# Performance work log

Hardware: AMD Instinct MI355X
Metric: run time of the kernel (lower is better)

The kernel has to match this reference:

```python
import jax, jax.numpy as jnp
from jax import lax
import numpy as np
import math

NUM_CLASSES = 1
IOU_THR = 0.5
SCORE_THR = 0.05
MAX_DET = 300
IMG_H = IMG_W = 640


def _base_anchors(base_size, ratios, scales):
    n = len(ratios) * len(scales)
    a = np.zeros((n, 4))
    a[:, 2:] = base_size * np.tile(scales, (2, len(ratios))).T
    areas = a[:, 2] * a[:, 3]
    a[:, 2] = np.sqrt(areas / np.repeat(ratios, len(scales)))
    a[:, 3] = a[:, 2] * np.repeat(ratios, len(scales))
    a[:, 0::2] -= np.tile(a[:, 2] * 0.5, (2, 1)).T
    a[:, 1::2] -= np.tile(a[:, 3] * 0.5, (2, 1)).T
    return a


def build_anchors(H, W):
    # standard RetinaNet anchors: levels 3..7, 3 ratios x 3 scales
    ratios = np.array([0.5, 1.0, 2.0])
    scales = np.array([2.0 ** 0, 2.0 ** (1.0 / 3.0), 2.0 ** (2.0 / 3.0)])
    out = []
    for l in (3, 4, 5, 6, 7):
        stride, base = 2 ** l, 2 ** (l + 2)
        ba = _base_anchors(base, ratios, scales)  # (9,4)
        fh, fw = (H + stride - 1) // stride, (W + stride - 1) // stride
        sx = (np.arange(fw) + 0.5) * stride
        sy = (np.arange(fh) + 0.5) * stride
        xx, yy = np.meshgrid(sx, sy)  # (fh, fw) row-major over (y, x) -> matches head NHWC flatten
        shifts = np.stack([xx.ravel(), yy.ravel(), xx.ravel(), yy.ravel()], 1)
        out.append((shifts[:, None, :] + ba[None, :, :]).reshape(-1, 4))
    return jnp.asarray(np.concatenate(out, 0), jnp.float32)


def conv3x3(x, w, b):
    y = lax.conv_general_dilated(x, w, (1, 1), 'SAME', dimension_numbers=('NCHW', 'OIHW', 'NCHW'))
    return y + b[None, :, None, None]


def run_head(feat, ws, bs, ow, ob):
    h = feat
    for k in range(ws.shape[0]):  # 4 shared conv+relu layers
        h = jax.nn.relu(conv3x3(h, ws[k], bs[k]))
    return conv3x3(h, ow, ob)


def decode_boxes(anchors, reg):
    w = anchors[:, 2] - anchors[:, 0]
    h = anchors[:, 3] - anchors[:, 1]
    cx = anchors[:, 0] + 0.5 * w
    cy = anchors[:, 1] + 0.5 * h
    pcx = cx + reg[:, 0] * 0.1 * w
    pcy = cy + reg[:, 1] * 0.1 * h
    pw = jnp.exp(reg[:, 2] * 0.2) * w
    ph = jnp.exp(reg[:, 3] * 0.2) * h
    return jnp.stack([pcx - 0.5 * pw, pcy - 0.5 * ph, pcx + 0.5 * pw, pcy + 0.5 * ph], 1)


def greedy_nms(boxes, scores):
    # fixed-size greedy NMS (jit-safe stand-in for torchvision.ops.nms), capped at MAX_DET
    s0 = jnp.where(scores > SCORE_THR, scores, -jnp.inf)
    areas = (boxes[:, 2] - boxes[:, 0]) * (boxes[:, 3] - boxes[:, 1])

    def body(i, carry):
        s, out_s, out_b = carry
        j = jnp.argmax(s)
        sj = s[j]
        keep = sj > -jnp.inf
        bj = boxes[j]
        xx1 = jnp.maximum(bj[0], boxes[:, 0])
        yy1 = jnp.maximum(bj[1], boxes[:, 1])
        xx2 = jnp.minimum(bj[2], boxes[:, 2])
        yy2 = jnp.minimum(bj[3], boxes[:, 3])
        inter = jnp.maximum(xx2 - xx1, 0.0) * jnp.maximum(yy2 - yy1, 0.0)
        iou = inter / (areas + areas[j] - inter + 1e-8)
        s = jnp.where(iou > IOU_THR, -jnp.inf, s)  # self-IoU == 1 also removes j
        out_s = out_s.at[i].set(jnp.where(keep, sj, 0.0))
        out_b = out_b.at[i].set(jnp.where(keep, bj, jnp.zeros((4,), boxes.dtype)))
        return s, out_s, out_b

    init = (s0, jnp.zeros((MAX_DET,), boxes.dtype), jnp.zeros((MAX_DET, 4), boxes.dtype))
    _, out_s, out_b = lax.fori_loop(0, MAX_DET, body, init)
    return out_s, out_b


def forward(img, feats, cls_w, cls_b, cls_ow, cls_ob, reg_w, reg_b, reg_ow, reg_ob):
    B = feats[0].shape[0]
    cls_list, reg_list = [], []
    for f in feats:
        c = run_head(f, cls_w, cls_b, cls_ow, cls_ob)  # [B, 9*C, h, w]
        cls_list.append(jnp.transpose(c, (0, 2, 3, 1)).reshape(B, -1, NUM_CLASSES))
        r = run_head(f, reg_w, reg_b, reg_ow, reg_ob)  # [B, 36, h, w]
        reg_list.append(jnp.transpose(r, (0, 2, 3, 1)).reshape(B, -1, 4))
    classification = jax.nn.sigmoid(jnp.concatenate(cls_list, 1))  # [B, N, C]
    regression = jnp.concatenate(reg_list, 1)                      # [B, N, 4]
    H, W = img.shape[2], img.shape[3]
    anchors = build_anchors(H, W)
    boxes = decode_boxes(anchors, regression[0])
    boxes = jnp.clip(boxes, jnp.zeros((4,), boxes.dtype), jnp.asarray([W, H, W, H], boxes.dtype))
    all_s, all_l, all_b = [], [], []
    for i in range(NUM_CLASSES):  # static per-class loop, mirrors eager loop
        s, b = greedy_nms(boxes, classification[0, :, i])
        all_s.append(s)
        all_b.append(b)
        all_l.append(jnp.where(s > 0.0, i, -1))
    return jnp.concatenate(all_s), jnp.concatenate(all_l), jnp.concatenate(all_b, 0)


def setup_inputs():
    key = jax.random.key(0)
    ks = jax.random.split(key, 16)
    C = 256
    scale = 0.03  # ~He std for 3x3x256 fan-in; keeps head activations O(1)
    sizes = [(80, 80), (40, 40), (20, 20), (10, 10), (5, 5)]
    inp = {'img': jnp.zeros((1, 3, IMG_H, IMG_W), jnp.float32)}
    for i, (name, (h, w)) in enumerate(zip(['p3', 'p4', 'p5', 'p6', 'p7'], sizes)):
        inp[name] = jax.random.normal(ks[i], (1, C, h, w), jnp.float32)
    na = 9
    bias_init = -math.log((1.0 - 0.01) / 0.01)  # prior_probability = 0.01
    inp['cls_w'] = jax.random.normal(ks[5], (4, C, C, 3, 3), jnp.float32) * scale
    inp['cls_b'] = jnp.zeros((4, C), jnp.float32)
    inp['cls_ow'] = jax.random.normal(ks[6], (na * NUM_CLASSES, C, 3, 3), jnp.float32) * scale
    inp['cls_ob'] = jnp.full((na * NUM_CLASSES,), bias_init, jnp.float32)
    inp['reg_w'] = jax.random.normal(ks[7], (4, C, C, 3, 3), jnp.float32) * scale
    inp['reg_b'] = jnp.zeros((4, C), jnp.float32)
    inp['reg_ow'] = jax.random.normal(ks[8], (na * 4, C, 3, 3), jnp.float32) * scale
    inp['reg_ob'] = jnp.zeros((na * 4,), jnp.float32)
    return inp


def reference(img, p3, p4, p5, p6, p7, cls_w, cls_b, cls_ow, cls_ob, reg_w, reg_b, reg_ow, reg_ob):
    return forward(img, (p3, p4, p5, p6, p7), cls_w, cls_b, cls_ow, cls_ob, reg_w, reg_b, reg_ow, reg_ob)
```

## Files before the change

kernel.cpp:

```cpp
#include <hip/hip_runtime.h>
#include <math.h>

#define N_ANCH 76725
#define SORT_N 4096
#define NBKT 1024
#define BBASE 0x3D40u

typedef _Float16 f16;
typedef _Float16 f16x8 __attribute__((ext_vector_type(8)));
typedef float f32x4 __attribute__((ext_vector_type(4)));

__device__ __forceinline__ int pick5(int l, int a, int b, int c, int d, int e) {
  int r = a;
  if (l == 1) r = b;
  if (l == 2) r = c;
  if (l == 3) r = d;
  if (l == 4) r = e;
  return r;
}

__device__ __forceinline__ void tile_to_level(int tile, int& lvl, int& t) {
  int l = 0;
  if (tile >= 100) l = 1;
  if (tile >= 125) l = 2;
  if (tile >= 134) l = 3;
  if (tile >= 138) l = 4;
  lvl = l;
  t = tile - pick5(l, 0, 100, 125, 134, 138);
}

__device__ __forceinline__ int tile64_lvl(int bx, int& t) {
  int l = 0;
  if (bx >= 100) l = 1;
  if (bx >= 125) l = 2;
  if (bx >= 132) l = 3;
  if (bx >= 134) l = 4;
  t = bx - pick5(l, 0, 100, 125, 132, 134);
  return l;
}

__device__ __forceinline__ void split16(float v, f16& h, f16& l) {
  f16 hh = (f16)v;
  if (fabsf(v) < 6.103515625e-5f) hh = (f16)0.f;
  h = hh;
  l = (f16)((v - (float)hh) * 4096.f);
}

__device__ __forceinline__ void glds16h(const void* g, void* l) {
  __builtin_amdgcn_global_load_lds(
      (const __attribute__((address_space(1))) unsigned int*)g,
      (__attribute__((address_space(3))) unsigned int*)l, 16, 0, 0);
}

__device__ __forceinline__ void glds16(const float* g, float* l) {
  __builtin_amdgcn_global_load_lds(
      (const __attribute__((address_space(1))) unsigned int*)g,
      (__attribute__((address_space(3))) unsigned int*)l, 16, 0, 0);
}

struct FcvArgs {
  const float* f[5];
  f16* hi;
  f16* lo;
  unsigned short* zbuf;
};

__global__ __launch_bounds__(256) void featcvt_k(FcvArgs a) {
  __shared__ float tile[32][65];
  int t;
  const int l = tile64_lvl(blockIdx.x, t);
  const int W = 80 >> l, HW = W * W;
  const int p0 = t * 64;
  const int apos = pick5(l, 0, 6400, 8000, 8400, 8500);
  const int ci0 = blockIdx.y * 32;
  const int tid = threadIdx.x;
  if (blockIdx.x == 0 && blockIdx.y == 0 && tid < 32) a.zbuf[tid] = 0;
  const float* __restrict__ src = a.f[l];
  #pragma unroll
  for (int i = 0; i < 8; i++) {
    const int j = tid + 256 * i;
    const int ci = j >> 6, p = j & 63;
    float v = 0.f;
    if (p0 + p < HW) v = src[(ci0 + ci) * HW + p0 + p];
    tile[ci][p] = v;
  }
  __syncthreads();
  const int p_l = tid >> 2, cq = tid & 3;
  if (p0 + p_l < HW) {
    union { f16 h[8]; uint4 v; } uh, ul;
    #pragma unroll
    for (int u = 0; u < 8; u++) split16(tile[cq * 8 + u][p_l], uh.h[u], ul.h[u]);
    const size_t base = (size_t)(apos + p0 + p_l) * 256 + ci0 + cq * 8;
    *(uint4*)(a.hi + base) = uh.v;
    *(uint4*)(a.lo + base) = ul.v;
  }
}

__global__ __launch_bounds__(256) void wsplit_k(const float* __restrict__ src,
                                                f16* __restrict__ whi,
                                                f16* __restrict__ wlo) {
  const int e = blockIdx.x * 256 + threadIdx.x;
  const int k = e & 31, co = (e >> 5) & 255, c = e >> 13;
  const int tap = c >> 3, ciq = c & 7;
  const int ci = ciq * 32 + k;
  const float v = src[((size_t)co * 256 + ci) * 9 + tap];
  f16 h, lo;
  split16(v, h, lo);
  whi[e] = h;
  wlo[e] = lo;
}

struct WtrArgs {
  const float* src[2];
  float* dst;
};

__global__ __launch_bounds__(256) void wtr_k(WtrArgs a) {
  __shared__ float tile[72][65];
  const int r0 = blockIdx.x * 72;
  const int cog = blockIdx.y;
  const int co0 = cog * 64;
  const int head = blockIdx.z;
  const float* __restrict__ src = a.src[head];
  float* __restrict__ dst = a.dst + ((size_t)(head * 4 + cog) * 2304 + r0) * 64;
  const int tid = threadIdx.x;
  #pragma unroll
  for (int i = 0; i < 18; i++) {
    int e = tid + 256 * i;
    int co = e / 72;
    int r = e - co * 72;
    tile[r][co] = src[(size_t)(co0 + co) * 2304 + r0 + r];
  }
  __syncthreads();
  #pragma unroll
  for (int i = 0; i < 18; i++) {
    int e = tid + 256 * i;
    int r = e >> 6;
    int co = e & 63;
    dst[(size_t)r * 64 + co] = tile[r][co];
  }
}

__device__ __forceinline__ void a_load(const float* __restrict__ in, int ci0,
                                       int ty0, int tx0, int W, int HW, int tid,
                                       float a_reg[6]) {
  const float* inc = in + ci0 * HW;
  #pragma unroll
  for (int i = 0; i < 6; i++) {
    int e = tid + 256 * i;
    float v = 0.f;
    if (e < 1440) {
      int ci = e / 180;
      int rem = e - ci * 180;
      int yy = rem / 10;
      int xx = rem - yy * 10;
      int gy = ty0 + yy - 1, gx = tx0 + xx - 1;
      if ((unsigned)gy < (unsigned)W && (unsigned)gx < (unsigned)W)
        v = inc[ci * HW + gy * W + gx];
    }
    a_reg[i] = v;
  }
}

__device__ __forceinline__ void a_store(int tid, const float a_reg[6],
                                        float As[8][18][12]) {
  #pragma unroll
  for (int i = 0; i < 6; i++) {
    int e = tid + 256 * i;
    if (e < 1440) {
      int ci = e / 180;
      int rem = e - ci * 180;
      int yy = rem / 10;
      int xx = rem - yy * 10;
      As[ci][yy][xx] = a_reg[i];
    }
  }
}

__device__ __forceinline__ void stage_w(const float* __restrict__ wchunk,
                                        float* wbuf, int wv, int lane) {
  #pragma unroll
  for (int i = 0; i < 5; i++) {
    int j = wv + 4 * i;
    if (j < 18) glds16(wchunk + j * 256 + lane * 4, wbuf + j * 256);
  }
}

struct FusedArgs {
  const f16* in_hi;
  const f16* in_lo;
  const f16* w_hi;
  const f16* w_lo;
  float* acc0;
  float* acc1;
  const f16* zbuf;
  const float* cin[5];
  float* cout[5];
  const float* cw;
  const float* cb;
};

__global__ __launch_bounds__(256, 2) void fused_trunk(FusedArgs a) {
  __shared__ __align__(16) char smem[65536];
  const int bx = blockIdx.x;
  const int tid = threadIdx.x;
  if (bx < 296) {
    f16 (*Xh)[4096] = (f16 (*)[4096])(smem);
    f16 (*Xl)[4096] = (f16 (*)[4096])(smem + 16384);
    f16 (*Wh)[4096] = (f16 (*)[4096])(smem + 32768);
    f16 (*Wl)[4096] = (f16 (*)[4096])(smem + 49152);
    const int combo = bx & 3, tl = bx >> 2;
    const int cog = combo >> 1, kh = combo & 1;
    int l = 0;
    if (tl >= 50) l = 1;
    if (tl >= 65) l = 2;
    if (tl >= 71) l = 3;
    if (tl >= 73) l = 4;
    const int t = tl - pick5(l, 0, 50, 65, 71, 73);
    const int W = 80 >> l, HW = W * W, tX = (W + 7) >> 3;
    const int ty0 = (t / tX) * 16, tx0 = (t % tX) * 8;
    const int apos = pick5(l, 0, 6400, 8000, 8400, 8500);
    const int co0 = cog * 128;
    const int lane = tid & 63, wv = tid >> 6;
    const int ln15 = lane & 15, lh = lane >> 4;
    const int wco = wv & 1, wpos = wv >> 1;
    const f16* __restrict__ ihi = a.in_hi;
    const f16* __restrict__ ilo = a.in_lo;
    const f16* __restrict__ whi = a.w_hi;
    const f16* __restrict__ wlo = a.w_lo;

    f32x4 accA[4][4] = {};
    f32x4 accB[4][4] = {};

    auto stage = [&](int c, int buf) {
      const int tap = c >> 3, ciq = c & 7;
      const int dy = tap / 3 - 1, dx = tap - (tap / 3) * 3 - 1;
      #pragma unroll
      for (int i = 0; i < 2; i++) {
        const int s = (wv * 2 + i) * 64 + lane;
        const int pos = s >> 2, kq = s & 3;
        const int kqd = kq ^ (pos & 3);
        const int gy = ty0 + (pos >> 3) + dy, gx = tx0 + (pos & 7) + dx;
        const bool v = (unsigned)gy < (unsigned)W && (unsigned)gx < (unsigned)W;
        const int off = (apos + gy * W + gx) * 256 + ciq * 32 + kqd * 8;
        glds16h(v ? (const void*)(ihi + off) : (const void*)a.zbuf, &Xh[buf][(wv * 2 + i) * 512]);
        glds16h(v ? (const void*)(ilo + off) : (const void*)a.zbuf, &Xl[buf][(wv * 2 + i) * 512]);
      }
      const f16* wh = whi + (size_t)c * 8192;
      const f16* wl = wlo + (size_t)c * 8192;
      #pragma unroll
      for (int i = 0; i < 2; i++) {
        const int s = (wv * 2 + i) * 64 + lane;
        const int col = s >> 2, kq = s & 3;
        const int kqd = kq ^ (col & 3);
        const int off = (co0 + col) * 32 + kqd * 8;
        glds16h(wh + off, &Wh[buf][(wv * 2 + i) * 512]);
        glds16h(wl + off, &Wl[buf][(wv * 2 + i) * 512]);
      }
    };

    const int c0 = kh * 36;
    stage(c0, 0);
    __syncthreads();
    for (int j = 0; j < 36; j++) {
      const int b = j & 1;
      if (j < 35) stage(c0 + j + 1, b ^ 1);
      const int slot = (lh ^ (ln15 & 3)) * 8;
      const int aro = (wco * 64 + ln15) * 32 + slot;
      const int bro = (wpos * 64 + ln15) * 32 + slot;
      f16x8 ah[4], al[4];
      #pragma unroll
      for (int mi = 0; mi < 4; mi++) {
        ah[mi] = *(const f16x8*)&Wh[b][aro + mi * 512];
        al[mi] = *(const f16x8*)&Wl[b][aro + mi * 512];
      }
      #pragma unroll
      for (int ni = 0; ni < 4; ni++) {
        const f16x8 bhv = *(const f16x8*)&Xh[b][bro + ni * 512];
        const f16x8 blv = *(const f16x8*)&Xl[b][bro + ni * 512];
        #pragma unroll
        for (int mi = 0; mi < 4; mi++) {
          accA[mi][ni] = __builtin_amdgcn_mfma_f32_16x16x32_f16(ah[mi], bhv, accA[mi][ni], 0, 0, 0);
          accB[mi][ni] = __builtin_amdgcn_mfma_f32_16x16x32_f16(ah[mi], blv, accB[mi][ni], 0, 0, 0);
          accB[mi][ni] = __builtin_amdgcn_mfma_f32_16x16x32_f16(al[mi], bhv, accB[mi][ni], 0, 0, 0);
        }
      }
      __syncthreads();
    }

    const int aoffF = pick5(l, 0, 1638400, 2048000, 2150400, 2176000);
    float* __restrict__ dst = (kh == 0 ? a.acc0 : a.acc1) + aoffF;
    #pragma unroll
    for (int ni = 0; ni < 4; ni++) {
      const int pos = wpos * 64 + ni * 16 + ln15;
      const int gy = ty0 + (pos >> 3), gx = tx0 + (pos & 7);
      if (gy < W && gx < W) {
        #pragma unroll
        for (int mi = 0; mi < 4; mi++) {
          const int co = co0 + wco * 64 + mi * 16 + lh * 4;
          float* d = dst + (size_t)co * HW + gy * W + gx;
          #pragma unroll
          for (int r = 0; r < 4; r++)
            d[(size_t)r * HW] = accA[mi][ni][r] + accB[mi][ni][r] * 2.44140625e-4f;
        }
      }
    }
  } else {
    float (*As)[8][18][12] = (float (*)[8][18][12])(smem);
    float (*Ws)[72][64] = (float (*)[72][64])(smem + 13824);
    const int idx = bx - 296;
    const int cog = idx & 3;
    const int tl = idx >> 2;
    int l = 0;
    if (tl >= 50) l = 1;
    if (tl >= 65) l = 2;
    if (tl >= 71) l = 3;
    if (tl >= 73) l = 4;
    const int lvl = l;
    const int t = tl - pick5(l, 0, 50, 65, 71, 73);
    const int W = 80 >> lvl;
    const int HW = W * W;
    const int tX = (W + 7) >> 3;
    const int ty0 = (t / tX) * 16, tx0 = (t % tX) * 8;
    const int co0 = cog << 6;
    const float* __restrict__ in = a.cin[lvl];
    float* __restrict__ out = a.cout[lvl];
    const float* __restrict__ wsrc = a.cw + (size_t)cog * 2304 * 64;
    const int lane = tid & 63, wv = tid >> 6;
    const int cop = tid & 15;
    const int ry = tid >> 4;
    const int co_sub = cop << 2;
    float acc[8][4] = {};
    float a_reg[6];

    stage_w(wsrc, &Ws[0][0][0], wv, lane);
    a_load(in, 0, ty0, tx0, W, HW, tid, a_reg);
    a_store(tid, a_reg, As[0]);
    __syncthreads();

    for (int k = 0; k < 32; k++) {
      const int kb = k & 1;
      const bool more = k < 31;
      if (more) {
        stage_w(wsrc + (size_t)(k + 1) * 4608, &Ws[kb ^ 1][0][0], wv, lane);
        a_load(in, (k + 1) * 8, ty0, tx0, W, HW, tid, a_reg);
      }
      #pragma unroll 2
      for (int ci = 0; ci < 8; ci++) {
        #pragma unroll
        for (int ty = 0; ty < 3; ty++) {
          const float* ar = &As[kb][ci][ry + ty][0];
          float4 a0 = *(const float4*)ar;
          float4 a1 = *(const float4*)(ar + 4);
          float2 a2 = *(const float2*)(ar + 8);
          float av[10] = {a0.x, a0.y, a0.z, a0.w, a1.x, a1.y, a1.z, a1.w, a2.x, a2.y};
          #pragma unroll
          for (int tx = 0; tx < 3; tx++) {
            const float* wr = &Ws[kb][ci * 9 + ty * 3 + tx][co_sub];
            float4 wvv = *(const float4*)wr;
            #pragma unroll
            for (int p = 0; p < 8; p++) {
              acc[p][0] = fmaf(av[tx + p], wvv.x, acc[p][0]);
              acc[p][1] = fmaf(av[tx + p], wvv.y, acc[p][1]);
              acc[p][2] = fmaf(av[tx + p], wvv.z, acc[p][2]);
              acc[p][3] = fmaf(av[tx + p], wvv.w, acc[p][3]);
            }
          }
        }
      }
      if (more) {
        a_store(tid, a_reg, As[kb ^ 1]);
        __syncthreads();
      }
    }
    const float4 bias = *(const float4*)&a.cb[co0 + co_sub];
    const int oy = ty0 + ry;
    if (oy < W) {
      #pragma unroll
      for (int p = 0; p < 8; p++) {
        int ox = tx0 + p;
        if (ox < W) {
          int base = oy * W + ox;
          out[(co0 + co_sub + 0) * HW + base] = fmaxf(acc[p][0] + bias.x, 0.f);
          out[(co0 + co_sub + 1) * HW + base] = fmaxf(acc[p][1] + bias.y, 0.f);
          out[(co0 + co_sub + 2) * HW + base] = fmaxf(acc[p][2] + bias.z, 0.f);
          out[(co0 + co_sub + 3) * HW + base] = fmaxf(acc[p][3] + bias.w, 0.f);
        }
      }
    }
  }
}

struct EpiArgs {
  float* a0;
  const float* a1;
  const float* bias;
  f16* hi;
  f16* lo;
  int last;
};

__global__ __launch_bounds__(256) void epi_k(EpiArgs a) {
  __shared__ float tile[32][65];
  int t;
  const int l = tile64_lvl(blockIdx.x, t);
  const int W = 80 >> l, HW = W * W;
  const int p0 = t * 64;
  const int apos = pick5(l, 0, 6400, 8000, 8400, 8500);
  const int ci0 = blockIdx.y * 32;
  const int tid = threadIdx.x;
  float* __restrict__ s0 = a.a0 + (size_t)apos * 256;
  const float* __restrict__ s1 = a.a1 + (size_t)apos * 256;
  const float* __restrict__ bias = a.bias;
  #pragma unroll
  for (int i = 0; i < 8; i++) {
    const int j = tid + 256 * i;
    const int ci = j >> 6, p = j & 63;
    float v = 0.f;
    if (p0 + p < HW) {
      const size_t off = (size_t)(ci0 + ci) * HW + p0 + p;
      float x = s0[off];
      float y = s1[off];
      v = x + y;
    }
    tile[ci][p] = fmaxf(v + bias[ci0 + ci], 0.f);
  }
  __syncthreads();
  if (a.last) {
    #pragma unroll
    for (int i = 0; i < 8; i++) {
      const int j = tid + 256 * i;
      const int ci = j >> 6, p = j & 63;
      if (p0 + p < HW) s0[(size_t)(ci0 + ci) * HW + p0 + p] = tile[ci][p];
    }
  } else {
    const int p_l = tid >> 2, cq = tid & 3;
    if (p0 + p_l < HW) {
      union { f16 h[8]; uint4 v; } uh, ul;
      #pragma unroll
      for (int u = 0; u < 8; u++) split16(tile[cq * 8 + u][p_l], uh.h[u], ul.h[u]);
      const size_t base = (size_t)(apos + p0 + p_l) * 256 + ci0 + cq * 8;
      *(uint4*)(a.hi + base) = uh.v;
      *(uint4*)(a.lo + base) = ul.v;
    }
  }
}

struct Out2Args {
  const float* in[2][5];
  const float* w;
  const float* b[2];
  float* dst[2];
};

__global__ __launch_bounds__(256) void wtro_k(const float* __restrict__ cls_ow,
                                              const float* __restrict__ reg_ow,
                                              float* __restrict__ dst) {
  int r = blockIdx.x * 256 + threadIdx.x;
  if (r >= 2304) return;
  for (int g = 0; g < 5; g++) {
    #pragma unroll
    for (int s = 0; s < 16; s++) {
      int w = s >> 2, c = s & 3;
      float v = 0.f;
      if (w < 3 && c < 3) {
        int cl = 3 * w + c;
        v = (g == 0) ? cls_ow[(size_t)cl * 2304 + r]
                     : reg_ow[(size_t)((g - 1) * 9 + cl) * 2304 + r];
      }
      dst[((size_t)g * 2304 + r) * 16 + s] = v;
    }
  }
}

__device__ __forceinline__ void ao_load(const float* __restrict__ in, int ci0,
                                        int ty0, int tx0, int W, int HW, int tid,
                                        float a_reg[5]) {
  const float* inc = in + ci0 * HW;
  #pragma unroll
  for (int i = 0; i < 5; i++) {
    int e = tid + 192 * i;
    float v = 0.f;
    if (e < 800) {
      int ci = e / 100;
      int rem = e - ci * 100;
      int yy = rem / 10;
      int xx = rem - yy * 10;
      int gy = ty0 + yy - 1, gx = tx0 + xx - 1;
      if ((unsigned)gy < (unsigned)W && (unsigned)gx < (unsigned)W)
        v = inc[ci * HW + gy * W + gx];
    }
    a_reg[i] = v;
  }
}

__device__ __forceinline__ void ao_store(int tid, const float a_reg[5],
                                         float As[8][10][12]) {
  #pragma unroll
  for (int i = 0; i < 5; i++) {
    int e = tid + 192 * i;
    if (e < 800) {
      int ci = e / 100;
      int rem = e - ci * 100;
      int yy = rem / 10;
      int xx = rem - yy * 10;
      As[ci][yy][xx] = a_reg[i];
    }
  }
}

__global__ __launch_bounds__(192) void conv_out2(Out2Args args) {
  __shared__ float As[2][8][10][12];
  __shared__ __align__(16) float Wg[2][8][9][16];
  int lvl, t;
  tile_to_level(blockIdx.x, lvl, t);
  const int g = blockIdx.y;
  const int head = (g == 0) ? 0 : 1;
  const int co0 = (g == 0) ? 0 : (g - 1) * 9;
  const int W = 80 >> lvl;
  const int HW = W * W;
  const int tX = (W + 7) >> 3;
  const int ty0 = (t / tX) * 8, tx0 = (t % tX) * 8;
  const float* __restrict__ in = args.in[head][lvl];
  const float* __restrict__ wg = args.w + (size_t)g * 2304 * 16;
  const int tid = threadIdx.x;
  const int wv = tid >> 6;
  const int lane = tid & 63;
  const int y = lane >> 3, x = lane & 7;
  float acc0 = 0.f, acc1 = 0.f, acc2 = 0.f;
  float a_reg[5];
  float4 w_reg[2];

  ao_load(in, 0, ty0, tx0, W, HW, tid, a_reg);
  {
    const float4* wsrc4 = (const float4*)wg;
    #pragma unroll
    for (int i = 0; i < 2; i++) {
      int e = tid + 192 * i;
      if (e < 288) w_reg[i] = wsrc4[e];
    }
  }
  ao_store(tid, a_reg, As[0]);
  {
    float4* wdst4 = (float4*)&Wg[0][0][0][0];
    #pragma unroll
    for (int i = 0; i < 2; i++) {
      int e = tid + 192 * i;
      if (e < 288) wdst4[e] = w_reg[i];
    }
  }
  __syncthreads();

  for (int k = 0; k < 32; k++) {
    const int kb = k & 1;
    const bool more = k < 31;
    if (more) {
      ao_load(in, (k + 1) * 8, ty0, tx0, W, HW, tid, a_reg);
      const float4* wsrc4 = (const float4*)(wg + (size_t)(k + 1) * 1152);
      #pragma unroll
      for (int i = 0; i < 2; i++) {
        int e = tid + 192 * i;
        if (e < 288) w_reg[i] = wsrc4[e];
      }
    }
    #pragma unroll 2
    for (int ci = 0; ci < 8; ci++) {
      #pragma unroll
      for (int ty = 0; ty < 3; ty++) {
        float a0 = As[kb][ci][y + ty][x + 0];
        float a1 = As[kb][ci][y + ty][x + 1];
        float a2 = As[kb][ci][y + ty][x + 2];
        #pragma unroll
        for (int tx = 0; tx < 3; tx++) {
          float av = (tx == 0) ? a0 : (tx == 1) ? a1 : a2;
          float4 w4 = *(const float4*)&Wg[kb][ci][ty * 3 + tx][4 * wv];
          acc0 = fmaf(av, w4.x, acc0);
          acc1 = fmaf(av, w4.y, acc1);
          acc2 = fmaf(av, w4.z, acc2);
        }
      }
    }
    if (more) {
      ao_store(tid, a_reg, As[kb ^ 1]);
      float4* wdst4 = (float4*)&Wg[kb ^ 1][0][0][0];
      #pragma unroll
      for (int i = 0; i < 2; i++) {
        int e = tid + 192 * i;
        if (e < 288) wdst4[e] = w_reg[i];
      }
      __syncthreads();
    }
  }
  const int oy = ty0 + y, ox = tx0 + x;
  if (oy < W && ox < W) {
    const int cell = oy * W + ox;
    const int aoff = pick5(lvl, 0, 57600, 72000, 75600, 76500);
    float* dst = args.dst[head];
    const float* bias = args.b[head];
    #pragma unroll
    for (int c = 0; c < 3; c++) {
      int co = co0 + 3 * wv + c;
      float v = ((c == 0) ? acc0 : (c == 1) ? acc1 : acc2) + bias[co];
      if (head == 0) {
        v = 1.f / (1.f + expf(-v));
        dst[aoff + cell * 9 + co] = v;
      } else {
        dst[(size_t)aoff * 4 + cell * 36 + co] = v;
      }
    }
  }
}

__global__ void init_k(int* meta) {
  int i = blockIdx.x * 256 + threadIdx.x;
  if (i < 1 + NBKT) meta[i] = 0;
}

__global__ __launch_bounds__(256) void decode_k(const float* __restrict__ scores,
                                                const float* __restrict__ regs,
                                                float* cand_s, float4* cand_b,
                                                int* cand_n, int* meta) {
  int n = blockIdx.x * 256 + threadIdx.x;
  if (n >= N_ANCH) return;
  int lvl = 0;
  if (n >= 57600) lvl = 1;
  if (n >= 72000) lvl = 2;
  if (n >= 75600) lvl = 3;
  if (n >= 76500) lvl = 4;
  const int aoff = pick5(lvl, 0, 57600, 72000, 75600, 76500);
  const int W = 80 >> lvl;
  int r = n - aoff;
  int a = r % 9;
  int cell = r / 9;
  int x = cell % W, y = cell / W;
  double stride = (double)(8 << lvl);
  double base = (double)(32 << lvl);
  int si = a % 3, ri = a / 3;
  double s = (si == 0) ? 1.0 : (si == 1) ? 1.2599210498948731648 : 1.5874010519681994748;
  double ratio = (ri == 0) ? 0.5 : (ri == 1) ? 1.0 : 2.0;
  double ws0 = base * s;
  double area = ws0 * ws0;
  double w = sqrt(area / ratio);
  double h = w * ratio;
  double cx = ((double)x + 0.5) * stride;
  double cy = ((double)y + 0.5) * stride;
  float ax1 = (float)(cx - 0.5 * w);
  float ay1 = (float)(cy - 0.5 * h);
  float ax2 = (float)(cx + (w - 0.5 * w));
  float ay2 = (float)(cy + (h - 0.5 * h));
  float4 rg = ((const float4*)regs)[n];
  float aw = ax2 - ax1, ah = ay2 - ay1;
  float acx = ax1 + 0.5f * aw, acy = ay1 + 0.5f * ah;
  float pcx = acx + rg.x * 0.1f * aw;
  float pcy = acy + rg.y * 0.1f * ah;
  float pw = expf(rg.z * 0.2f) * aw;
  float ph = expf(rg.w * 0.2f) * ah;
  float x1 = pcx - 0.5f * pw, y1 = pcy - 0.5f * ph;
  float x2 = pcx + 0.5f * pw, y2 = pcy + 0.5f * ph;
  x1 = fminf(fmaxf(x1, 0.f), 640.f);
  y1 = fminf(fmaxf(y1, 0.f), 640.f);
  x2 = fminf(fmaxf(x2, 0.f), 640.f);
  y2 = fminf(fmaxf(y2, 0.f), 640.f);
  float sc = scores[n];
  if (sc > 0.05f) {
    int p = atomicAdd(&meta[0], 1);
    cand_s[p] = sc;
    cand_b[p] = make_float4(x1, y1, x2, y2);
    cand_n[p] = n;
    unsigned int sb = __float_as_uint(sc);
    int bk = (int)(sb >> 16) - (int)BBASE;
    bk = max(0, min(NBKT - 1, bk));
    atomicAdd(&meta[1 + bk], 1);
  }
}

__global__ __launch_bounds__(1024) void nms2_k(const float* __restrict__ cs,
                                               const float4* __restrict__ cb,
                                               const int* __restrict__ cn,
                                               const int* __restrict__ meta,
                                               float* __restrict__ out) {
  __shared__ unsigned long long skey[SORT_N];
  __shared__ int sidx[SORT_N];
  __shared__ int suf[NBKT];
  __shared__ float kx1[300], ky1[300], kx2[300], ky2[300], kar[300];
  __shared__ int sh_i[8];
  const int tid = threadIdx.x;
  const int m = min(meta[0], N_ANCH);

  for (int b = tid; b < NBKT; b += 1024) suf[b] = meta[1 + b];
  __syncthreads();
  for (int off = 1; off < NBKT; off <<= 1) {
    int v0 = suf[tid] + ((tid + off < NBKT) ? suf[tid + off] : 0);
    __syncthreads();
    suf[tid] = v0;
    __syncthreads();
  }

  int nk = 0;
  unsigned long long hi64 = ~0ULL;
  int processed = 0;

  while (nk < 300 && processed < m) {
    int base = 0;
    if (hi64 != ~0ULL) {
      if (tid == 0) sh_i[4] = 0;
      __syncthreads();
      int c = 0;
      for (int j = tid; j < m; j += 1024) {
        unsigned long long K = ((unsigned long long)__float_as_uint(cs[j]) << 32) |
                               (unsigned int)(~cn[j]);
        if (K >= hi64) c++;
      }
      atomicAdd(&sh_i[4], c);
      __syncthreads();
      base = sh_i[4];
      __syncthreads();
    }
    if (tid == 0) sh_i[3] = NBKT + 1;
    __syncthreads();
    {
      int T = tid;
      unsigned long long lo =
          (T == 0) ? 0ULL : ((unsigned long long)(((unsigned)T + BBASE) << 16) << 32);
      int c = suf[T] - base;
      if (lo < hi64 && c >= 1 && c <= SORT_N) atomicMin(&sh_i[3], T);
    }
    __syncthreads();
    int T = sh_i[3];
    __syncthreads();
    unsigned long long lo64;
    if (T <= NBKT) {
      lo64 = (T == 0) ? 0ULL : ((unsigned long long)(((unsigned)T + BBASE) << 16) << 32);
    } else {
      unsigned long long L = 0, H = hi64;
      while (H - L > 1) {
        unsigned long long mid = L + ((H - L) >> 1);
        if (tid == 0) sh_i[4] = 0;
        __syncthreads();
        int c = 0;
        for (int j = tid; j < m; j += 1024) {
          unsigned long long K = ((unsigned long long)__float_as_uint(cs[j]) << 32) |
                                 (unsigned int)(~cn[j]);
          if (K >= mid && K < hi64) c++;
        }
        atomicAdd(&sh_i[4], c);
        __syncthreads();
        int cc = sh_i[4];
        __syncthreads();
        if (cc > SORT_N) L = mid; else H = mid;
      }
      lo64 = H;
    }
    if (tid == 0) sh_i[0] = 0;
    __syncthreads();
    for (int j = tid; j < m; j += 1024) {
      unsigned long long K = ((unsigned long long)__float_as_uint(cs[j]) << 32) |
                             (unsigned int)(~cn[j]);
      if (K >= lo64 && K < hi64) {
        int p = atomicAdd(&sh_i[0], 1);
        if (p < SORT_N) { skey[p] = K; sidx[p] = j; }
      }
    }
    __syncthreads();
    int bn = min(sh_i[0], SORT_N);
    __syncthreads();
    for (int p = bn + tid; p < SORT_N; p += 1024) { skey[p] = 0; sidx[p] = 0; }
    __syncthreads();
    for (int k = 2; k <= SORT_N; k <<= 1) {
      for (int jj = k >> 1; jj > 0; jj >>= 1) {
        for (int i = tid; i < SORT_N; i += 1024) {
          int l2 = i ^ jj;
          if (l2 > i) {
            unsigned long long a = skey[i], b2 = skey[l2];
            bool desc = ((i & k) == 0);
            if ((a < b2) == desc) {
              skey[i] = b2; skey[l2] = a;
              int t2 = sidx[i]; sidx[i] = sidx[l2]; sidx[l2] = t2;
            }
          }
        }
        __syncthreads();
      }
    }
    {
      char* pool = (char*)skey;
      float* cx1 = (float*)pool;
      float* cy1 = cx1 + 256;
      float* cx2 = cy1 + 256;
      float* cy2 = cx2 + 256;
      float* car = cy2 + 256;
      int* sup = (int*)(car + 256);
      unsigned long long* msk = (unsigned long long*)(pool + 6144);
      int cpos = 0;
      while (cpos < bn && nk < 300) {
        const int cl = min(256, bn - cpos);
        if (tid < 256) sup[tid] = 0;
        if (tid < cl) {
          float4 b = cb[sidx[cpos + tid]];
          cx1[tid] = b.x; cy1[tid] = b.y; cx2[tid] = b.z; cy2[tid] = b.w;
          car[tid] = (b.z - b.x) * (b.w - b.y);
        }
        __syncthreads();
        {
          const int i = tid >> 2, q = tid & 3;
          if (i < cl) {
            const float bx1 = cx1[i], by1 = cy1[i], bx2 = cx2[i], by2 = cy2[i], ba = car[i];
            int flag = 0;
            for (int k2 = q; k2 < nk; k2 += 4) {
              float xx1 = fmaxf(kx1[k2], bx1), yy1 = fmaxf(ky1[k2], by1);
              float xx2 = fminf(kx2[k2], bx2), yy2 = fminf(ky2[k2], by2);
              float inter = fmaxf(xx2 - xx1, 0.f) * fmaxf(yy2 - yy1, 0.f);
              if (inter / (ba + kar[k2] - inter + 1e-8f) > 0.5f) { flag = 1; break; }
            }
            if (flag) atomicOr(&sup[i], 1);
          }
        }
        {
          const int i = tid >> 2, w = tid & 3;
          unsigned long long bits = 0ull;
          if (i < cl) {
            const float ax1 = cx1[i], ay1 = cy1[i], ax2 = cx2[i], ay2 = cy2[i], aa = car[i];
            const int j0 = w * 64;
            for (int jj = 0; jj < 64; jj++) {
              const int j2 = j0 + jj;
              if (j2 > i && j2 < cl) {
                float xx1 = fmaxf(ax1, cx1[j2]), yy1 = fmaxf(ay1, cy1[j2]);
                float xx2 = fminf(ax2, cx2[j2]), yy2 = fminf(ay2, cy2[j2]);
                float inter = fmaxf(xx2 - xx1, 0.f) * fmaxf(yy2 - yy1, 0.f);
                if (inter / (car[j2] + aa - inter + 1e-8f) > 0.5f) bits |= (1ull << jj);
              }
            }
          }
          msk[(tid >> 2) * 4 + (tid & 3)] = bits;
        }
        __syncthreads();
        if (tid == 0) {
          unsigned long long r0 = 0, r1 = 0, r2 = 0, r3 = 0;
          int lnk = nk;
          for (int i = 0; i < cl && lnk < 300; i++) {
            const unsigned long long rw = (i < 64) ? r0 : (i < 128) ? r1 : (i < 192) ? r2 : r3;
            if (sup[i] || ((rw >> (i & 63)) & 1ull)) continue;
            const float b1 = cx1[i], b2 = cy1[i], b3 = cx2[i], b4 = cy2[i];
            kx1[lnk] = b1; ky1[lnk] = b2; kx2[lnk] = b3; ky2[lnk] = b4; kar[lnk] = car[i];
            out[lnk] = cs[sidx[cpos + i]];
            out[300 + lnk] = 0.0f;
            out[600 + 4 * lnk + 0] = b1;
            out[600 + 4 * lnk + 1] = b2;
            out[600 + 4 * lnk + 2] = b3;
            out[600 + 4 * lnk + 3] = b4;
            lnk++;
            r0 |= msk[i * 4 + 0]; r1 |= msk[i * 4 + 1];
            r2 |= msk[i * 4 + 2]; r3 |= msk[i * 4 + 3];
          }
          sh_i[5] = lnk;
        }
        __syncthreads();
        nk = sh_i[5];
        cpos += cl;
        __syncthreads();
      }
    }
    processed = base + bn;
    hi64 = lo64;
  }
  __syncthreads();
  for (int r = nk + tid; r < 300; r += 1024) {
    out[r] = 0.f;
    out[300 + r] = -1.f;
    out[600 + 4 * r + 0] = 0.f;
    out[600 + 4 * r + 1] = 0.f;
    out[600 + 4 * r + 2] = 0.f;
    out[600 + 4 * r + 3] = 0.f;
  }
}

extern "C" void kernel_launch(void* const* d_in, const int* in_sizes, int n_in,
                              void* d_out, int out_size, void* d_ws, size_t ws_size,
                              hipStream_t stream) {
  (void)in_sizes; (void)n_in; (void)out_size; (void)ws_size;
  const float* feats[5];
  for (int ll = 0; ll < 5; ll++) feats[ll] = (const float*)d_in[1 + ll];
  const float* cls_w = (const float*)d_in[6];
  const float* cls_b = (const float*)d_in[7];
  const float* cls_ow = (const float*)d_in[8];
  const float* cls_ob = (const float*)d_in[9];
  const float* reg_w = (const float*)d_in[10];
  const float* reg_b = (const float*)d_in[11];
  const float* reg_ow = (const float*)d_in[12];
  const float* reg_ob = (const float*)d_in[13];

  static const int AOFF[5] = {0, 1638400, 2048000, 2150400, 2176000};
  const size_t ACT = 2182400;
  const size_t PLH = 2182400;

  float* wsf = (float*)d_ws;
  float* ACC0 = wsf;
  float* ACC1 = wsf + ACT;
  float* clsA = wsf + 2 * ACT;
  float* clsB = wsf + 3 * ACT;
  f16* slotA = (f16*)(wsf + 4 * ACT);
  f16* slotB = (f16*)(wsf + 5 * ACT);
  float* wt = wsf + 6 * ACT;
  f16* wpkh = (f16*)(wsf + 6 * ACT + 589824);
  f16* wpkl = (f16*)(wsf + 6 * ACT + 884736);
  unsigned short* zbuf = (unsigned short*)(wsf + 6 * ACT + 1179648);
  float* scores = wsf + 6 * ACT + 1179664;
  float* regs = scores + 76736;
  float* cand_s = regs + 306912;
  float* cand_b = cand_s + 76736;
  int* cand_n = (int*)(cand_b + 306944);
  int* meta = cand_n + 76736;
  float* wt2o = (float*)(meta + 1032);

  FcvArgs fa;
  for (int ll = 0; ll < 5; ll++) fa.f[ll] = feats[ll];
  fa.hi = slotB;
  fa.lo = slotB + PLH;
  fa.zbuf = zbuf;
  featcvt_k<<<dim3(135, 8), dim3(256), 0, stream>>>(fa);
  wtro_k<<<dim3(9), dim3(256), 0, stream>>>(cls_ow, reg_ow, wt2o);

  float* clsBufs[2] = {clsA, clsB};
  for (int layer = 0; layer < 4; layer++) {
    wsplit_k<<<dim3(2304), dim3(256), 0, stream>>>(reg_w + (size_t)layer * 589824, wpkh, wpkl);
    WtrArgs wa;
    wa.src[0] = cls_w + (size_t)layer * 589824;
    wa.src[1] = wa.src[0];
    wa.dst = wt;
    wtr_k<<<dim3(32, 4, 1), dim3(256), 0, stream>>>(wa);

    FusedArgs fu;
    if (layer == 0) {
      fu.in_hi = slotB;
      fu.in_lo = slotB + PLH;
    } else {
      f16* s = (layer & 1) ? slotA : slotB;
      fu.in_hi = s;
      fu.in_lo = s + PLH;
    }
    fu.w_hi = wpkh;
    fu.w_lo = wpkl;
    fu.acc0 = ACC0;
    fu.acc1 = ACC1;
    fu.zbuf = (const f16*)zbuf;
    fu.cw = wt;
    fu.cb = cls_b + layer * 256;
    for (int ll = 0; ll < 5; ll++) {
      fu.cout[ll] = clsBufs[layer & 1] + AOFF[ll];
      fu.cin[ll] = (layer == 0) ? feats[ll]
                                : (const float*)(clsBufs[(layer - 1) & 1] + AOFF[ll]);
    }
    fused_trunk<<<dim3(592), dim3(256), 0, stream>>>(fu);

    EpiArgs ea;
    f16* outS = (layer & 1) ? slotB : slotA;
    ea.a0 = ACC0;
    ea.a1 = ACC1;
    ea.bias = reg_b + layer * 256;
    ea.hi = outS;
    ea.lo = outS + PLH;
    ea.last = (layer == 3) ? 1 : 0;
    epi_k<<<dim3(135, 8), dim3(256), 0, stream>>>(ea);
  }

  Out2Args oa;
  for (int ll = 0; ll < 5; ll++) {
    oa.in[0][ll] = clsB + AOFF[ll];
    oa.in[1][ll] = ACC0 + AOFF[ll];
  }
  oa.w = wt2o;
  oa.b[0] = cls_ob;
  oa.b[1] = reg_ob;
  oa.dst[0] = scores;
  oa.dst[1] = regs;
  conv_out2<<<dim3(139, 5), dim3(192), 0, stream>>>(oa);

  init_k<<<dim3(5), dim3(256), 0, stream>>>(meta);
  decode_k<<<dim3((N_ANCH + 255) / 256), dim3(256), 0, stream>>>(scores, regs, cand_s,
                                                                 (float4*)cand_b, cand_n, meta);
  nms2_k<<<dim3(1), dim3(1024), 0, stream>>>(cand_s, (const float4*)cand_b, cand_n, meta,
                                             (float*)d_out);
}
```

Measured before the change: 1.422 ms.

## Hoist weight prep out of layer loop and split cls conv blocks finer

All four layers' weight split and transpose now run in one launch each before the layer loop, removing eight small launches from the loop. The fp32 cls-head conv blocks now cover 32 output channels and half-width columns instead of 64, and fused_trunk grows from 592 to 888 blocks. Cls and reg blocks are interleaved in a 1:2 ratio so the two kinds of work mix across CUs. Each cls block does less work with fewer accumulator registers, which adds parallelism but reloads activations twice as often and stores less reuse per block.

```diff
diff --git a/kernel.cpp b/kernel.cpp
--- a/kernel.cpp
+++ b/kernel.cpp
@@ -96,22 +96,24 @@
   }
 }
 
-__global__ __launch_bounds__(256) void wsplit_k(const float* __restrict__ src,
+__global__ __launch_bounds__(256) void wsplit_k(const float* __restrict__ reg_w,
                                                 f16* __restrict__ whi,
                                                 f16* __restrict__ wlo) {
   const int e = blockIdx.x * 256 + threadIdx.x;
+  const int layer = blockIdx.y;
+  const float* src = reg_w + (size_t)layer * 589824;
   const int k = e & 31, co = (e >> 5) & 255, c = e >> 13;
   const int tap = c >> 3, ciq = c & 7;
   const int ci = ciq * 32 + k;
   const float v = src[((size_t)co * 256 + ci) * 9 + tap];
   f16 h, lo;
   split16(v, h, lo);
-  whi[e] = h;
-  wlo[e] = lo;
+  whi[(size_t)layer * 589824 + e] = h;
+  wlo[(size_t)layer * 589824 + e] = lo;
 }
 
 struct WtrArgs {
-  const float* src[2];
+  const float* src;
   float* dst;
 };
 
@@ -120,9 +122,9 @@
   const int r0 = blockIdx.x * 72;
   const int cog = blockIdx.y;
   const int co0 = cog * 64;
-  const int head = blockIdx.z;
-  const float* __restrict__ src = a.src[head];
-  float* __restrict__ dst = a.dst + ((size_t)(head * 4 + cog) * 2304 + r0) * 64;
+  const int layer = blockIdx.z;
+  const float* __restrict__ src = a.src + (size_t)layer * 589824;
+  float* __restrict__ dst = a.dst + (size_t)layer * 589824 + ((size_t)cog * 2304 + r0) * 64;
   const int tid = threadIdx.x;
   #pragma unroll
   for (int i = 0; i < 18; i++) {
@@ -177,15 +179,6 @@
   }
 }
 
-__device__ __forceinline__ void stage_w(const float* __restrict__ wchunk,
-                                        float* wbuf, int wv, int lane) {
-  #pragma unroll
-  for (int i = 0; i < 5; i++) {
-    int j = wv + 4 * i;
-    if (j < 18) glds16(wchunk + j * 256 + lane * 4, wbuf + j * 256);
-  }
-}
-
 struct FusedArgs {
   const f16* in_hi;
   const f16* in_lo;
@@ -204,12 +197,14 @@
   __shared__ __align__(16) char smem[65536];
   const int bx = blockIdx.x;
   const int tid = threadIdx.x;
-  if (bx < 296) {
+  const int q3 = bx / 3, r3 = bx - q3 * 3;
+  if (r3 == 0) {
     f16 (*Xh)[4096] = (f16 (*)[4096])(smem);
     f16 (*Xl)[4096] = (f16 (*)[4096])(smem + 16384);
     f16 (*Wh)[4096] = (f16 (*)[4096])(smem + 32768);
     f16 (*Wl)[4096] = (f16 (*)[4096])(smem + 49152);
-    const int combo = bx & 3, tl = bx >> 2;
+    const int rb = q3;
+    const int combo = rb & 3, tl = rb >> 2;
     const int cog = combo >> 1, kh = combo & 1;
     int l = 0;
     if (tl >= 50) l = 1;
@@ -307,10 +302,10 @@
     }
   } else {
     float (*As)[8][18][12] = (float (*)[8][18][12])(smem);
-    float (*Ws)[72][64] = (float (*)[72][64])(smem + 13824);
-    const int idx = bx - 296;
-    const int cog = idx & 3;
-    const int tl = idx >> 2;
+    float (*Ws)[72][32] = (float (*)[72][32])(smem + 13824);
+    const int cls_idx = q3 * 2 + (r3 - 1);
+    const int cog = cls_idx & 7;
+    const int tl = cls_idx >> 3;
     int l = 0;
     if (tl >= 50) l = 1;
     if (tl >= 65) l = 2;
@@ -322,18 +317,30 @@
     const int HW = W * W;
     const int tX = (W + 7) >> 3;
     const int ty0 = (t / tX) * 16, tx0 = (t % tX) * 8;
-    const int co0 = cog << 6;
+    const int co0 = cog << 5;
+    const int cog64 = cog >> 1, half = cog & 1;
     const float* __restrict__ in = a.cin[lvl];
     float* __restrict__ out = a.cout[lvl];
-    const float* __restrict__ wsrc = a.cw + (size_t)cog * 2304 * 64;
+    const float* __restrict__ wsrc = a.cw + (size_t)cog64 * 2304 * 64;
     const int lane = tid & 63, wv = tid >> 6;
-    const int cop = tid & 15;
+    const int cop = tid & 7;
     const int ry = tid >> 4;
-    const int co_sub = cop << 2;
-    float acc[8][4] = {};
+    const int xh = (tid >> 3) & 1;
+    float acc[4][4] = {};
     float a_reg[6];
 
-    stage_w(wsrc, &Ws[0][0][0], wv, lane);
+    auto stage32 = [&](const float* wchunk, float* wbuf) {
+      #pragma unroll
+      for (int i2 = 0; i2 < 3; i2++) {
+        int j = wv + 4 * i2;
+        if (j < 9) {
+          const float* src = wchunk + (j * 8 + (lane >> 3)) * 64 + half * 32 + (lane & 7) * 4;
+          glds16(src, wbuf + j * 256);
+        }
+      }
+    };
+
+    stage32(wsrc, &Ws[0][0][0]);
     a_load(in, 0, ty0, tx0, W, HW, tid, a_reg);
     a_store(tid, a_reg, As[0]);
     __syncthreads();
@@ -342,28 +349,26 @@
       const int kb = k & 1;
       const bool more = k < 31;
       if (more) {
-        stage_w(wsrc + (size_t)(k + 1) * 4608, &Ws[kb ^ 1][0][0], wv, lane);
+        stage32(wsrc + (size_t)(k + 1) * 4608, &Ws[kb ^ 1][0][0]);
         a_load(in, (k + 1) * 8, ty0, tx0, W, HW, tid, a_reg);
       }
       #pragma unroll 2
       for (int ci = 0; ci < 8; ci++) {
         #pragma unroll
         for (int ty = 0; ty < 3; ty++) {
-          const float* ar = &As[kb][ci][ry + ty][0];
+          const float* ar = &As[kb][ci][ry + ty][xh * 4];
           float4 a0 = *(const float4*)ar;
-          float4 a1 = *(const float4*)(ar + 4);
-          float2 a2 = *(const float2*)(ar + 8);
-          float av[10] = {a0.x, a0.y, a0.z, a0.w, a1.x, a1.y, a1.z, a1.w, a2.x, a2.y};
+          float2 a1 = *(const float2*)(ar + 4);
+          float av[6] = {a0.x, a0.y, a0.z, a0.w, a1.x, a1.y};
           #pragma unroll
           for (int tx = 0; tx < 3; tx++) {
-            const float* wr = &Ws[kb][ci * 9 + ty * 3 + tx][co_sub];
-            float4 wvv = *(const float4*)wr;
+            float4 w4 = *(const float4*)&Ws[kb][ci * 9 + ty * 3 + tx][cop * 4];
             #pragma unroll
-            for (int p = 0; p < 8; p++) {
-              acc[p][0] = fmaf(av[tx + p], wvv.x, acc[p][0]);
-              acc[p][1] = fmaf(av[tx + p], wvv.y, acc[p][1]);
-              acc[p][2] = fmaf(av[tx + p], wvv.z, acc[p][2]);
-              acc[p][3] = fmaf(av[tx + p], wvv.w, acc[p][3]);
+            for (int p = 0; p < 4; p++) {
+              acc[p][0] = fmaf(av[tx + p], w4.x, acc[p][0]);
+              acc[p][1] = fmaf(av[tx + p], w4.y, acc[p][1]);
+              acc[p][2] = fmaf(av[tx + p], w4.z, acc[p][2]);
+              acc[p][3] = fmaf(av[tx + p], w4.w, acc[p][3]);
             }
           }
         }
@@ -373,18 +378,18 @@
         __syncthreads();
       }
     }
-    const float4 bias = *(const float4*)&a.cb[co0 + co_sub];
+    const float4 bias = *(const float4*)&a.cb[co0 + cop * 4];
     const int oy = ty0 + ry;
     if (oy < W) {
       #pragma unroll
-      for (int p = 0; p < 8; p++) {
-        int ox = tx0 + p;
+      for (int p = 0; p < 4; p++) {
+        int ox = tx0 + xh * 4 + p;
         if (ox < W) {
           int base = oy * W + ox;
-          out[(co0 + co_sub + 0) * HW + base] = fmaxf(acc[p][0] + bias.x, 0.f);
-          out[(co0 + co_sub + 1) * HW + base] = fmaxf(acc[p][1] + bias.y, 0.f);
-          out[(co0 + co_sub + 2) * HW + base] = fmaxf(acc[p][2] + bias.z, 0.f);
-          out[(co0 + co_sub + 3) * HW + base] = fmaxf(acc[p][3] + bias.w, 0.f);
+          out[(co0 + cop * 4 + 0) * HW + base] = fmaxf(acc[p][0] + bias.x, 0.f);
+          out[(co0 + cop * 4 + 1) * HW + base] = fmaxf(acc[p][1] + bias.y, 0.f);
+          out[(co0 + cop * 4 + 2) * HW + base] = fmaxf(acc[p][2] + bias.z, 0.f);
+          out[(co0 + cop * 4 + 3) * HW + base] = fmaxf(acc[p][3] + bias.w, 0.f);
         }
       }
     }
@@ -835,10 +840,10 @@
         }
         __syncthreads();
         if (tid == 0) {
-          unsigned long long r0 = 0, r1 = 0, r2 = 0, r3 = 0;
+          unsigned long long r0 = 0, r1 = 0, r2 = 0, r3b = 0;
           int lnk = nk;
           for (int i = 0; i < cl && lnk < 300; i++) {
-            const unsigned long long rw = (i < 64) ? r0 : (i < 128) ? r1 : (i < 192) ? r2 : r3;
+            const unsigned long long rw = (i < 64) ? r0 : (i < 128) ? r1 : (i < 192) ? r2 : r3b;
             if (sup[i] || ((rw >> (i & 63)) & 1ull)) continue;
             const float b1 = cx1[i], b2 = cy1[i], b3 = cx2[i], b4 = cy2[i];
             kx1[lnk] = b1; ky1[lnk] = b2; kx2[lnk] = b3; ky2[lnk] = b4; kar[lnk] = car[i];
@@ -850,7 +855,7 @@
             out[600 + 4 * lnk + 3] = b4;
             lnk++;
             r0 |= msk[i * 4 + 0]; r1 |= msk[i * 4 + 1];
-            r2 |= msk[i * 4 + 2]; r3 |= msk[i * 4 + 3];
+            r2 |= msk[i * 4 + 2]; r3b |= msk[i * 4 + 3];
           }
           sh_i[5] = lnk;
         }
@@ -900,11 +905,11 @@
   float* clsB = wsf + 3 * ACT;
   f16* slotA = (f16*)(wsf + 4 * ACT);
   f16* slotB = (f16*)(wsf + 5 * ACT);
-  float* wt = wsf + 6 * ACT;
-  f16* wpkh = (f16*)(wsf + 6 * ACT + 589824);
-  f16* wpkl = (f16*)(wsf + 6 * ACT + 884736);
-  unsigned short* zbuf = (unsigned short*)(wsf + 6 * ACT + 1179648);
-  float* scores = wsf + 6 * ACT + 1179664;
+  float* wt4 = wsf + 6 * ACT;
+  f16* wpkh4 = (f16*)(wsf + 6 * ACT + 2359296);
+  f16* wpkl4 = (f16*)(wsf + 6 * ACT + 3538944);
+  unsigned short* zbuf = (unsigned short*)(wsf + 6 * ACT + 4718592);
+  float* scores = wsf + 6 * ACT + 4718608;
   float* regs = scores + 76736;
   float* cand_s = regs + 306912;
   float* cand_b = cand_s + 76736;
@@ -919,16 +924,14 @@
   fa.zbuf = zbuf;
   featcvt_k<<<dim3(135, 8), dim3(256), 0, stream>>>(fa);
   wtro_k<<<dim3(9), dim3(256), 0, stream>>>(cls_ow, reg_ow, wt2o);
+  wsplit_k<<<dim3(2304, 4), dim3(256), 0, stream>>>(reg_w, wpkh4, wpkl4);
+  WtrArgs wa;
+  wa.src = cls_w;
+  wa.dst = wt4;
+  wtr_k<<<dim3(32, 4, 4), dim3(256), 0, stream>>>(wa);
 
   float* clsBufs[2] = {clsA, clsB};
   for (int layer = 0; layer < 4; layer++) {
-    wsplit_k<<<dim3(2304), dim3(256), 0, stream>>>(reg_w + (size_t)layer * 589824, wpkh, wpkl);
-    WtrArgs wa;
-    wa.src[0] = cls_w + (size_t)layer * 589824;
-    wa.src[1] = wa.src[0];
-    wa.dst = wt;
-    wtr_k<<<dim3(32, 4, 1), dim3(256), 0, stream>>>(wa);
-
     FusedArgs fu;
     if (layer == 0) {
       fu.in_hi = slotB;
@@ -938,19 +941,19 @@
       fu.in_hi = s;
       fu.in_lo = s + PLH;
     }
-    fu.w_hi = wpkh;
-    fu.w_lo = wpkl;
+    fu.w_hi = wpkh4 + (size_t)layer * 589824;
+    fu.w_lo = wpkl4 + (size_t)layer * 589824;
     fu.acc0 = ACC0;
     fu.acc1 = ACC1;
     fu.zbuf = (const f16*)zbuf;
-    fu.cw = wt;
+    fu.cw = wt4 + (size_t)layer * 589824;
     fu.cb = cls_b + layer * 256;
     for (int ll = 0; ll < 5; ll++) {
       fu.cout[ll] = clsBufs[layer & 1] + AOFF[ll];
       fu.cin[ll] = (layer == 0) ? feats[ll]
                                 : (const float*)(clsBufs[(layer - 1) & 1] + AOFF[ll]);
     }
-    fused_trunk<<<dim3(592), dim3(256), 0, stream>>>(fu);
+    fused_trunk<<<dim3(888), dim3(256), 0, stream>>>(fu);
 
     EpiArgs ea;
     f16* outS = (layer & 1) ? slotB : slotA;
```

Result: faster. 1.375 ms (median of 2 runs) (-3.2%).
